# Kernel optimization log

Measured on AMD Instinct MI355X. Metric: run time of the kernel, lower is better.

The kernel has to match this reference:

```python
import jax, jax.numpy as jnp
import numpy as np

B, N, L, H, D = 4, 256, 4, 256, 128  # batch, nodes, labels, hidden, hidden//2
DEG = 16                              # neighbors per (label, node) row (fixed by construction)
M = L * DEG                           # == max_neighbor in the torch code (total degree)


def setup_inputs() -> dict:
    key = jax.random.key(0)
    ks = jax.random.split(key, 12)
    x = jax.random.normal(ks[0], (B, N, H), dtype=jnp.float32)
    feature = jax.random.normal(ks[1], (B, N, 2), dtype=jnp.float32)
    # adjacency with exactly DEG neighbors per (b, l, k) row -> max_neighbor = L*DEG static
    scores = jax.random.uniform(ks[2], (B, L, N, N), dtype=jnp.float32)
    nb = jnp.argsort(-scores, axis=-1)[..., :DEG]                     # [B,L,N,DEG]
    adj = jax.nn.one_hot(nb, N, dtype=jnp.float32).sum(axis=-2)      # [B,L,N,N] binary
    # parameters
    fc_w = jax.random.normal(ks[3], (H, H + 2), dtype=jnp.float32) / np.sqrt(H + 2)
    fc_b = jnp.zeros((H,), jnp.float32)
    ln_g = jnp.ones((H,), jnp.float32)
    ln_b = jnp.zeros((H,), jnp.float32)
    W = jax.random.normal(ks[4], (L, H, D), dtype=jnp.float32) * np.sqrt(2.0 / (H + D))  # xavier
    w_ih = jax.random.normal(ks[5], (4 * H, D), dtype=jnp.float32) / np.sqrt(H)
    w_hh = jax.random.normal(ks[6], (4 * H, H), dtype=jnp.float32) / np.sqrt(H)
    b_ih = jnp.zeros((4 * H,), jnp.float32)
    b_hh = jnp.zeros((4 * H,), jnp.float32)
    return dict(x=x, feature=feature, adj=adj, fc_w=fc_w, fc_b=fc_b, ln_g=ln_g,
                ln_b=ln_b, W=W, w_ih=w_ih, w_hh=w_hh, b_ih=b_ih, b_hh=b_hh)


def _lstm_last(seq, w_ih, w_hh, b_ih, b_hh):
    # seq: [Bt, T, D]; torch nn.LSTM gate order (i, f, g, o); returns last hidden [Bt, Hh]
    Bt = seq.shape[0]
    Hh = w_hh.shape[1]
    bias = b_ih + b_hh

    def step(carry, xt):
        h, c = carry
        gates = xt @ w_ih.T + h @ w_hh.T + bias          # [Bt, 4H]
        i, f, g, o = jnp.split(gates, 4, axis=-1)
        c = jax.nn.sigmoid(f) * c + jax.nn.sigmoid(i) * jnp.tanh(g)
        h = jax.nn.sigmoid(o) * jnp.tanh(c)
        return (h, c), None

    h0 = jnp.zeros((Bt, Hh), seq.dtype)
    (h, _), _ = jax.lax.scan(step, (h0, h0), jnp.swapaxes(seq, 0, 1))
    return h


def reference(x, feature, adj, fc_w, fc_b, ln_g, ln_b, W, w_ih, w_hh, b_ih, b_hh):
    # fc + layernorm + tanh (dropout: eval mode -> identity)
    h = jnp.concatenate([x, feature], axis=-1) @ fc_w.T + fc_b        # [B,N,H]
    mu = h.mean(-1, keepdims=True)
    var = h.var(-1, keepdims=True)
    h = (h - mu) / jnp.sqrt(var + 1e-5) * ln_g + ln_b
    h = jnp.tanh(h)
    # per-label projection of all node features: xw[b,l,n] = h[b,n] @ W[l]
    xw = jnp.einsum('bnh,lhd->blnd', h, W)                            # [B,L,N,D]
    # packed neighbor indices in ascending node order (argsort is stable; adj binary)
    idx = jnp.argsort(1.0 - adj, axis=-1)[..., :DEG]                  # [B,L,N,DEG]
    neigh = jnp.take_along_axis(xw[:, :, None, :, :], idx[..., None], axis=3)  # [B,L,N,DEG,D]
    # torch fills only first deg slots per label, zero-pads to max_neighbor = M
    supports = jnp.pad(neigh, ((0, 0), (0, 0), (0, 0), (0, M - DEG), (0, 0)))  # [B,L,N,M,D]
    supports = jnp.transpose(supports, (0, 2, 1, 3, 4)).reshape(-1, M, xw.shape[-1])  # [B*N*L,M,D]
    last = _lstm_last(supports, w_ih, w_hh, b_ih, b_hh).reshape(h.shape[0], h.shape[1], L, -1)
    out = h + last.mean(axis=2)
    return out + h   # returned dict['x'] = 2*h + mean(supports)
```

## Files before the change

### kernel.cpp

```cpp
#include <hip/hip_runtime.h>
#include <hip/hip_bf16.h>
#include <math.h>

#define B_ 4
#define N_ 256
#define L_ 4
#define H_ 256
#define D_ 128
#define DEG_ 16
#define T_ 64

#define OFF_H     0
#define OFF_FCWT  262144
#define OFF_BIAS  328192
#define OFF_IDX   329216
#define OFF_XWB   394752
#define OFF_PHH   656896
#define OFF_PIH   787968
#define OFF_HG    853504
#define OFF_CTR   1902080

typedef __attribute__((ext_vector_type(8))) short short8;
typedef __attribute__((ext_vector_type(4))) float f32x4;

__device__ __forceinline__ float sigf(float x)  { return 1.f / (1.f + __expf(-x)); }
__device__ __forceinline__ float tanhf_(float x){ return 2.f / (1.f + __expf(-2.f * x)) - 1.f; }
__device__ __forceinline__ unsigned short f2b(float f) {
    __hip_bfloat16 h = __float2bfloat16(f);
    return __builtin_bit_cast(unsigned short, h);
}
__device__ __forceinline__ float b2f(unsigned short s) {
    unsigned int u = ((unsigned int)s) << 16;
    return __builtin_bit_cast(float, u);
}
__device__ __forceinline__ f32x4 splat4(float v) { f32x4 r; r[0]=v; r[1]=v; r[2]=v; r[3]=v; return r; }

__global__ void k_prep(const float* __restrict__ fc_w, const float* __restrict__ w_ih,
                       const float* __restrict__ w_hh, const float* __restrict__ b_ih,
                       const float* __restrict__ b_hh, float* __restrict__ ws) {
    int i = blockIdx.x * blockDim.x + threadIdx.x;
    unsigned short* phh = (unsigned short*)(ws + OFF_PHH);
    unsigned short* pih = (unsigned short*)(ws + OFF_PIH);
    if (i < 256) ((int*)(ws + OFF_CTR))[i] = 0;
    if (i < 66048) {
        int k = i >> 8, j = i & 255;
        ws[OFF_FCWT + i] = fc_w[j * 258 + k];
    } else if (i < 66048 + 262144) {
        int p = i - 66048;
        int j = p & 7, lane = (p >> 3) & 63, kt = (p >> 9) & 7, nt = (p >> 12) & 3, w = (p >> 14) & 7, slc = (p >> 17) & 1;
        int n = nt * 256 + slc * 128 + w * 16 + (lane & 15);
        int k = kt * 32 + (lane >> 4) * 8 + j;
        phh[p] = f2b(w_hh[n * 256 + k]);
    } else if (i < 66048 + 262144 + 131072) {
        int p = i - (66048 + 262144);
        int j = p & 7, lane = (p >> 3) & 63, kt = (p >> 9) & 3, nt = (p >> 11) & 3, w = (p >> 13) & 7, slc = (p >> 16) & 1;
        int n = nt * 256 + slc * 128 + w * 16 + (lane & 15);
        int k = kt * 32 + (lane >> 4) * 8 + j;
        pih[p] = f2b(w_ih[n * 128 + k]);
    } else if (i < 66048 + 262144 + 131072 + 1024) {
        int u = i - (66048 + 262144 + 131072);
        ws[OFF_BIAS + u] = b_ih[u] + b_hh[u];
    }
}

__global__ void k_fc_ln(const float* __restrict__ x, const float* __restrict__ feat,
                        const float* __restrict__ fc_b, const float* __restrict__ ln_g,
                        const float* __restrict__ ln_b, float* __restrict__ ws) {
    __shared__ float inl[260];
    __shared__ float r1[256], r2[256];
    int row = blockIdx.x, tid = threadIdx.x;
    inl[tid] = x[row * H_ + tid];
    if (tid < 2) inl[H_ + tid] = feat[row * 2 + tid];
    __syncthreads();
    const float* fcwT = ws + OFF_FCWT;
    float acc = fc_b[tid];
    #pragma unroll 4
    for (int k = 0; k < 258; ++k) acc += fcwT[k * 256 + tid] * inl[k];
    r1[tid] = acc; r2[tid] = acc * acc;
    __syncthreads();
    for (int o = 128; o > 0; o >>= 1) {
        if (tid < o) { r1[tid] += r1[tid + o]; r2[tid] += r2[tid + o]; }
        __syncthreads();
    }
    float mu  = r1[0] * (1.f / 256.f);
    float var = r2[0] * (1.f / 256.f) - mu * mu;
    float v = (acc - mu) * rsqrtf(var + 1e-5f) * ln_g[tid] + ln_b[tid];
    ws[OFF_H + row * H_ + tid] = tanhf_(v);
}

__global__ void k_xw(const float* __restrict__ Wm, float* __restrict__ ws) {
    __shared__ float hs[32 * 256];
    int bid = blockIdx.x;
    int tile = bid & 7, l = (bid >> 3) & 3, b = bid >> 5;
    int n0 = tile * 32, tid = threadIdx.x;
    const float* hsrc = ws + OFF_H + (b * N_ + n0) * H_;
    for (int i = tid * 4; i < 32 * 256; i += 256 * 4)
        *(float4*)&hs[i] = *(const float4*)&hsrc[i];
    __syncthreads();
    int r0 = (tid >> 5) * 4, c0 = (tid & 31) * 4;
    float acc[4][4] = {};
    const float* wl = Wm + l * H_ * D_;
    for (int k = 0; k < 256; ++k) {
        float4 wv = *(const float4*)&wl[k * D_ + c0];
        #pragma unroll
        for (int r = 0; r < 4; ++r) {
            float hv = hs[(r0 + r) * 256 + k];
            acc[r][0] += hv * wv.x; acc[r][1] += hv * wv.y;
            acc[r][2] += hv * wv.z; acc[r][3] += hv * wv.w;
        }
    }
    unsigned short* xwb = (unsigned short*)(ws + OFF_XWB);
    #pragma unroll
    for (int r = 0; r < 4; ++r) {
        unsigned int lo = (unsigned int)f2b(acc[r][0]) | ((unsigned int)f2b(acc[r][1]) << 16);
        unsigned int hi = (unsigned int)f2b(acc[r][2]) | ((unsigned int)f2b(acc[r][3]) << 16);
        uint2 v; v.x = lo; v.y = hi;
        *(uint2*)&xwb[((b * L_ + l) * N_ + (n0 + r0 + r)) * D_ + c0] = v;
    }
}

__global__ void k_idx(const float* __restrict__ adj, float* __restrict__ ws) {
    int row = blockIdx.x;
    int tid = threadIdx.x;
    __shared__ int wc[4];
    bool a = adj[row * N_ + tid] > 0.5f;
    unsigned long long m = __ballot(a);
    int lane = tid & 63, w = tid >> 6;
    if (lane == 0) wc[w] = __popcll(m);
    __syncthreads();
    int base = 0;
    for (int i = 0; i < w; ++i) base += wc[i];
    int pos = base + __popcll(m & ((1ull << lane) - 1ull));
    int* idxb = (int*)(ws + OFF_IDX);
    if (a && pos < DEG_) idxb[row * DEG_ + pos] = tid;
}

__global__ __launch_bounds__(512, 2)
void k_lstm2(float* __restrict__ out, float* __restrict__ ws) {
    __shared__ __align__(16) unsigned short wih_s[65536];
    __shared__ __align__(16) unsigned short hbuf[32 * 256];
    __shared__ int idx_s[32 * 16];
    const int tid = threadIdx.x;
    const int lane = tid & 63, w = tid >> 6;
    const int c15 = lane & 15, lg = lane >> 4;
    const int bid = blockIdx.x;
    const int g = (bid & 7) | ((bid >> 4) << 3);
    const int slc = (bid >> 3) & 1;
    const int partner = bid ^ 8;
    const int gs0 = g * 32;

    const unsigned short* phh = (const unsigned short*)(ws + OFF_PHH);
    const unsigned short* pih = (const unsigned short*)(ws + OFF_PIH);
    const float* bias = ws + OFF_BIAS;
    const int* idxb = (const int*)(ws + OFF_IDX);
    const unsigned short* xwb = (const unsigned short*)(ws + OFF_XWB);
    unsigned short* hg = (unsigned short*)(ws + OFF_HG);
    int* ctr = (int*)(ws + OFF_CTR);

    {
        const uint4* src = (const uint4*)(pih + slc * 65536);
        uint4* dst = (uint4*)wih_s;
        for (int i = tid; i < 8192; i += 512) dst[i] = src[i];
    }
    for (int i = tid; i < 4096; i += 512) ((unsigned int*)hbuf)[i] = 0;
    {
        int sl = tid >> 4, tt = tid & 15;
        int gsq = gs0 + sl;
        int bbx = gsq >> 10, nn = (gsq >> 2) & 255, ll = gsq & 3;
        idx_s[sl * 16 + tt] = idxb[(((bbx << 2) + ll) * 256 + nn) * DEG_ + tt];
    }

    short8 WH[4][8];
    const short8* ph8 = (const short8*)phh;
    #pragma unroll
    for (int nt = 0; nt < 4; ++nt)
        #pragma unroll
        for (int kt = 0; kt < 8; ++kt)
            WH[nt][kt] = ph8[(((slc * 8 + w) * 32) + nt * 8 + kt) * 64 + lane];

    float bb4[4];
    #pragma unroll
    for (int nt = 0; nt < 4; ++nt) bb4[nt] = bias[nt * 256 + slc * 128 + w * 16 + c15];

    int xbb[2];
    #pragma unroll
    for (int m = 0; m < 2; ++m) {
        int gsq = gs0 + m * 16 + c15;
        int bbx = gsq >> 10, ll = gsq & 3;
        xbb[m] = ((bbx << 2) + ll) * 256;
    }

    float cst[2][4];
    #pragma unroll
    for (int m = 0; m < 2; ++m)
        #pragma unroll
        for (int r = 0; r < 4; ++r) cst[m][r] = 0.f;

    const int sr = tid >> 4, sch = tid & 15;
    const int slcP = 1 - slc;

    __syncthreads();

    for (int t = 0; t < T_; ++t) {
        const int cur = t & 1, nxt = cur ^ 1;
        if (t > 0) {
            if (tid == 0) {
                while (__hip_atomic_load(ctr + partner, __ATOMIC_RELAXED, __HIP_MEMORY_SCOPE_AGENT) < t)
                    __builtin_amdgcn_s_sleep(1);
            }
            __syncthreads();
            {
                const unsigned long long* src = (const unsigned long long*)
                    (hg + ((long)(g * 2 + cur) * 32 + sr) * 256 + slcP * 128 + sch * 8);
                unsigned long long v0 = __hip_atomic_load(src,     __ATOMIC_RELAXED, __HIP_MEMORY_SCOPE_AGENT);
                unsigned long long v1 = __hip_atomic_load(src + 1, __ATOMIC_RELAXED, __HIP_MEMORY_SCOPE_AGENT);
                unsigned short* d = hbuf + sr * 256 + (((slcP * 16 + sch) ^ (sr & 7)) * 8);
                *(unsigned long long*)d = v0;
                *(unsigned long long*)(d + 4) = v1;
            }
            __syncthreads();
        }

        float hv[2][4];
        #pragma unroll
        for (int m = 0; m < 2; ++m) {
            short8 hA[8];
            #pragma unroll
            for (int kt = 0; kt < 8; ++kt)
                hA[kt] = *(const short8*)&hbuf[(m * 16 + c15) * 256 + (((kt * 4 + lg) ^ (c15 & 7)) * 8)];
            short8 xA[4];
            if (t < DEG_) {
                int nb = idx_s[(m * 16 + c15) * 16 + t];
                const short8* s8 = (const short8*)(xwb + (xbb[m] + nb) * D_);
                #pragma unroll
                for (int kt = 0; kt < 4; ++kt) xA[kt] = s8[kt * 4 + lg];
            }
            f32x4 acc[4];
            #pragma unroll
            for (int nt = 0; nt < 4; ++nt) {
                acc[nt] = splat4(bb4[nt]);
                #pragma unroll
                for (int kt = 0; kt < 8; ++kt)
                    acc[nt] = __builtin_amdgcn_mfma_f32_16x16x32_bf16(hA[kt], WH[nt][kt], acc[nt], 0, 0, 0);
                if (t < DEG_) {
                    #pragma unroll
                    for (int kt = 0; kt < 4; ++kt) {
                        short8 wf = *(const short8*)&wih_s[(((w * 4 + nt) * 4 + kt) * 64 + lane) * 8];
                        acc[nt] = __builtin_amdgcn_mfma_f32_16x16x32_bf16(xA[kt], wf, acc[nt], 0, 0, 0);
                    }
                }
            }
            #pragma unroll
            for (int r = 0; r < 4; ++r) {
                float gi = sigf(acc[0][r]);
                float gf = sigf(acc[1][r]);
                float gg = tanhf_(acc[2][r]);
                float go = sigf(acc[3][r]);
                float cc = gf * cst[m][r] + gi * gg;
                cst[m][r] = cc;
                hv[m][r] = go * tanhf_(cc);
            }
        }
        __syncthreads();
        #pragma unroll
        for (int m = 0; m < 2; ++m)
            #pragma unroll
            for (int r = 0; r < 4; ++r) {
                int row = m * 16 + lg * 4 + r;
                int cu = slc * 128 + w * 16 + c15;
                int chunk = (cu >> 3) ^ (row & 7);
                hbuf[row * 256 + chunk * 8 + (c15 & 7)] = f2b(hv[m][r]);
            }
        __syncthreads();
        if (t < T_ - 1) {
            const unsigned short* s = hbuf + sr * 256 + (((slc * 16 + sch) ^ (sr & 7)) * 8);
            unsigned long long v0 = *(const unsigned long long*)s;
            unsigned long long v1 = *(const unsigned long long*)(s + 4);
            unsigned long long* d = (unsigned long long*)
                (hg + ((long)(g * 2 + nxt) * 32 + sr) * 256 + slc * 128 + sch * 8);
            __hip_atomic_store(d,     v0, __ATOMIC_RELAXED, __HIP_MEMORY_SCOPE_AGENT);
            __hip_atomic_store(d + 1, v1, __ATOMIC_RELAXED, __HIP_MEMORY_SCOPE_AGENT);
            __syncthreads();
            if (tid == 0)
                __hip_atomic_store(ctr + bid, t + 1, __ATOMIC_RELAXED, __HIP_MEMORY_SCOPE_AGENT);
        }
    }

    const float* hln = ws + OFF_H;
    const int p = tid >> 6, uu = tid & 63;
    const int bn = g * 8 + p;
    #pragma unroll
    for (int j = 0; j < 2; ++j) {
        int cu = slc * 128 + j * 64 + uu;
        float ssum = 0.f;
        #pragma unroll
        for (int l2 = 0; l2 < 4; ++l2) {
            int s = p * 4 + l2;
            ssum += b2f(hbuf[s * 256 + (((cu >> 3) ^ (s & 7)) * 8) + (cu & 7)]);
        }
        int gi = bn * 256 + cu;
        out[gi] = 2.f * hln[gi] + 0.25f * ssum;
    }
}

extern "C" void kernel_launch(void* const* d_in, const int* in_sizes, int n_in,
                              void* d_out, int out_size, void* d_ws, size_t ws_size,
                              hipStream_t stream) {
    const float* x    = (const float*)d_in[0];
    const float* feat = (const float*)d_in[1];
    const float* adj  = (const float*)d_in[2];
    const float* fc_w = (const float*)d_in[3];
    const float* fc_b = (const float*)d_in[4];
    const float* ln_g = (const float*)d_in[5];
    const float* ln_b = (const float*)d_in[6];
    const float* Wm   = (const float*)d_in[7];
    const float* w_ih = (const float*)d_in[8];
    const float* w_hh = (const float*)d_in[9];
    const float* b_ih = (const float*)d_in[10];
    const float* b_hh = (const float*)d_in[11];
    float* ws  = (float*)d_ws;
    float* out = (float*)d_out;

    hipLaunchKernelGGL(k_prep,   dim3(1798), dim3(256), 0, stream, fc_w, w_ih, w_hh, b_ih, b_hh, ws);
    hipLaunchKernelGGL(k_fc_ln,  dim3(1024), dim3(256), 0, stream, x, feat, fc_b, ln_g, ln_b, ws);
    hipLaunchKernelGGL(k_xw,     dim3(128),  dim3(256), 0, stream, Wm, ws);
    hipLaunchKernelGGL(k_idx,    dim3(4096), dim3(256), 0, stream, adj, ws);
    hipLaunchKernelGGL(k_lstm2,  dim3(256),  dim3(512), 0, stream, out, ws);
}
```

Baseline: 411.1 us.

## Read partner half of hidden state directly from global, drop LDS staging barrier

Each block of the pair no longer copies the partner's half of the hidden state into shared memory behind an extra barrier each step. It loads those four K-tiles straight from the global exchange buffer into MFMA operands, and rotates the W_hh K-tile order so its own half comes from LDS. This removes one __syncthreads and an LDS round trip per timestep on the serial LSTM critical path. In exchange, the exchange buffer and counters are zeroed with a memset so step-0 global reads are valid, which adds an extra memset launch.

```diff
diff --git a/kernel.cpp b/kernel.cpp
--- a/kernel.cpp
+++ b/kernel.cpp
@@ -35,13 +35,19 @@
 }
 __device__ __forceinline__ f32x4 splat4(float v) { f32x4 r; r[0]=v; r[1]=v; r[2]=v; r[3]=v; return r; }
 
+__device__ __forceinline__ short8 ld_hg16(const unsigned short* p) {
+    union { unsigned long long q[2]; short8 s; } u;
+    u.q[0] = __hip_atomic_load((const unsigned long long*)p,     __ATOMIC_RELAXED, __HIP_MEMORY_SCOPE_AGENT);
+    u.q[1] = __hip_atomic_load(((const unsigned long long*)p) + 1, __ATOMIC_RELAXED, __HIP_MEMORY_SCOPE_AGENT);
+    return u.s;
+}
+
 __global__ void k_prep(const float* __restrict__ fc_w, const float* __restrict__ w_ih,
                        const float* __restrict__ w_hh, const float* __restrict__ b_ih,
                        const float* __restrict__ b_hh, float* __restrict__ ws) {
     int i = blockIdx.x * blockDim.x + threadIdx.x;
     unsigned short* phh = (unsigned short*)(ws + OFF_PHH);
     unsigned short* pih = (unsigned short*)(ws + OFF_PIH);
-    if (i < 256) ((int*)(ws + OFF_CTR))[i] = 0;
     if (i < 66048) {
         int k = i >> 8, j = i & 255;
         ws[OFF_FCWT + i] = fc_w[j * 258 + k];
@@ -147,6 +153,7 @@
     const int g = (bid & 7) | ((bid >> 4) << 3);
     const int slc = (bid >> 3) & 1;
     const int partner = bid ^ 8;
+    const int ktO = slc * 4;
     const int gs0 = g * 32;
 
     const unsigned short* phh = (const unsigned short*)(ws + OFF_PHH);
@@ -175,8 +182,10 @@
     #pragma unroll
     for (int nt = 0; nt < 4; ++nt)
         #pragma unroll
-        for (int kt = 0; kt < 8; ++kt)
-            WH[nt][kt] = ph8[(((slc * 8 + w) * 32) + nt * 8 + kt) * 64 + lane];
+        for (int kk = 0; kk < 8; ++kk) {
+            int pkt = (ktO + kk) & 7;
+            WH[nt][kk] = ph8[(((slc * 8 + w) * 32) + nt * 8 + pkt) * 64 + lane];
+        }
 
     float bb4[4];
     #pragma unroll
@@ -189,6 +198,7 @@
         int bbx = gsq >> 10, ll = gsq & 3;
         xbb[m] = ((bbx << 2) + ll) * 256;
     }
+    const int slcP = 1 - slc;
 
     float cst[2][4];
     #pragma unroll
@@ -197,7 +207,6 @@
         for (int r = 0; r < 4; ++r) cst[m][r] = 0.f;
 
     const int sr = tid >> 4, sch = tid & 15;
-    const int slcP = 1 - slc;
 
     __syncthreads();
 
@@ -209,25 +218,21 @@
                     __builtin_amdgcn_s_sleep(1);
             }
             __syncthreads();
-            {
-                const unsigned long long* src = (const unsigned long long*)
-                    (hg + ((long)(g * 2 + cur) * 32 + sr) * 256 + slcP * 128 + sch * 8);
-                unsigned long long v0 = __hip_atomic_load(src,     __ATOMIC_RELAXED, __HIP_MEMORY_SCOPE_AGENT);
-                unsigned long long v1 = __hip_atomic_load(src + 1, __ATOMIC_RELAXED, __HIP_MEMORY_SCOPE_AGENT);
-                unsigned short* d = hbuf + sr * 256 + (((slcP * 16 + sch) ^ (sr & 7)) * 8);
-                *(unsigned long long*)d = v0;
-                *(unsigned long long*)(d + 4) = v1;
-            }
-            __syncthreads();
         }
 
         float hv[2][4];
         #pragma unroll
         for (int m = 0; m < 2; ++m) {
             short8 hA[8];
+            {
+                const unsigned short* prow = hg + ((long)(g * 2 + cur) * 32 + (m * 16 + c15)) * 256 + slcP * 128;
+                #pragma unroll
+                for (int kk = 4; kk < 8; ++kk)
+                    hA[kk] = ld_hg16(prow + ((kk - 4) * 4 + lg) * 8);
+            }
             #pragma unroll
-            for (int kt = 0; kt < 8; ++kt)
-                hA[kt] = *(const short8*)&hbuf[(m * 16 + c15) * 256 + (((kt * 4 + lg) ^ (c15 & 7)) * 8)];
+            for (int kk = 0; kk < 4; ++kk)
+                hA[kk] = *(const short8*)&hbuf[(m * 16 + c15) * 256 + ((((ktO + kk) * 4 + lg) ^ (c15 & 7)) * 8)];
             short8 xA[4];
             if (t < DEG_) {
                 int nb = idx_s[(m * 16 + c15) * 16 + t];
@@ -240,8 +245,8 @@
             for (int nt = 0; nt < 4; ++nt) {
                 acc[nt] = splat4(bb4[nt]);
                 #pragma unroll
-                for (int kt = 0; kt < 8; ++kt)
-                    acc[nt] = __builtin_amdgcn_mfma_f32_16x16x32_bf16(hA[kt], WH[nt][kt], acc[nt], 0, 0, 0);
+                for (int kk = 0; kk < 8; ++kk)
+                    acc[nt] = __builtin_amdgcn_mfma_f32_16x16x32_bf16(hA[kk], WH[nt][kk], acc[nt], 0, 0, 0);
                 if (t < DEG_) {
                     #pragma unroll
                     for (int kt = 0; kt < 4; ++kt) {
@@ -321,6 +326,8 @@
     float* ws  = (float*)d_ws;
     float* out = (float*)d_out;
 
+    hipMemsetAsync((char*)d_ws + (size_t)OFF_HG * 4, 0,
+                   (size_t)(OFF_CTR + 256 - OFF_HG) * 4, stream);
     hipLaunchKernelGGL(k_prep,   dim3(1798), dim3(256), 0, stream, fc_w, w_ih, w_hh, b_ih, b_hh, ws);
     hipLaunchKernelGGL(k_fc_ln,  dim3(1024), dim3(256), 0, stream, x, feat, fc_b, ln_g, ln_b, ws);
     hipLaunchKernelGGL(k_xw,     dim3(128),  dim3(256), 0, stream, Wm, ws);
```

New measurement: 563.7 us. 37.1% more time.

## Fuse neighbor-index extraction into LSTM kernel and split recurrence loop

Applied to the files above, without the earlier changes.

Drops the separate k_idx launch and builds each row's packed neighbor indices inside the LSTM kernel, using wave ballots over the adjacency rows. The time loop is split into a first phase with input projection (t<DEG) and a second phase without it, which removes the per-step branch. Each thread now writes its hidden values straight to global memory before the LDS write, so the extra copy pass and the barrier before the partner signal go away. The cost is more adjacency reads at the start of the LSTM kernel, and the partner sync now depends on element-wise relaxed atomic stores followed by barriers.

```diff
diff --git a/kernel.cpp b/kernel.cpp
--- a/kernel.cpp
+++ b/kernel.cpp
@@ -13,7 +13,6 @@
 #define OFF_H     0
 #define OFF_FCWT  262144
 #define OFF_BIAS  328192
-#define OFF_IDX   329216
 #define OFF_XWB   394752
 #define OFF_PHH   656896
 #define OFF_PIH   787968
@@ -119,24 +118,8 @@
     }
 }
 
-__global__ void k_idx(const float* __restrict__ adj, float* __restrict__ ws) {
-    int row = blockIdx.x;
-    int tid = threadIdx.x;
-    __shared__ int wc[4];
-    bool a = adj[row * N_ + tid] > 0.5f;
-    unsigned long long m = __ballot(a);
-    int lane = tid & 63, w = tid >> 6;
-    if (lane == 0) wc[w] = __popcll(m);
-    __syncthreads();
-    int base = 0;
-    for (int i = 0; i < w; ++i) base += wc[i];
-    int pos = base + __popcll(m & ((1ull << lane) - 1ull));
-    int* idxb = (int*)(ws + OFF_IDX);
-    if (a && pos < DEG_) idxb[row * DEG_ + pos] = tid;
-}
-
 __global__ __launch_bounds__(512, 2)
-void k_lstm2(float* __restrict__ out, float* __restrict__ ws) {
+void k_lstm2(const float* __restrict__ adj, float* __restrict__ out, float* __restrict__ ws) {
     __shared__ __align__(16) unsigned short wih_s[65536];
     __shared__ __align__(16) unsigned short hbuf[32 * 256];
     __shared__ int idx_s[32 * 16];
@@ -148,11 +131,10 @@
     const int slc = (bid >> 3) & 1;
     const int partner = bid ^ 8;
     const int gs0 = g * 32;
-
-    const unsigned short* phh = (const unsigned short*)(ws + OFF_PHH);
+    const int cu0 = slc * 128 + w * 16 + c15;
+
     const unsigned short* pih = (const unsigned short*)(ws + OFF_PIH);
     const float* bias = ws + OFF_BIAS;
-    const int* idxb = (const int*)(ws + OFF_IDX);
     const unsigned short* xwb = (const unsigned short*)(ws + OFF_XWB);
     unsigned short* hg = (unsigned short*)(ws + OFF_HG);
     int* ctr = (int*)(ws + OFF_CTR);
@@ -163,15 +145,25 @@
         for (int i = tid; i < 8192; i += 512) dst[i] = src[i];
     }
     for (int i = tid; i < 4096; i += 512) ((unsigned int*)hbuf)[i] = 0;
-    {
-        int sl = tid >> 4, tt = tid & 15;
+    #pragma unroll
+    for (int q = 0; q < 4; ++q) {
+        int sl = w * 4 + q;
         int gsq = gs0 + sl;
         int bbx = gsq >> 10, nn = (gsq >> 2) & 255, ll = gsq & 3;
-        idx_s[sl * 16 + tt] = idxb[(((bbx << 2) + ll) * 256 + nn) * DEG_ + tt];
+        const float* arow = adj + ((size_t)((((bbx << 2) + ll) * 256 + nn))) * 256;
+        int base = 0;
+        #pragma unroll
+        for (int j = 0; j < 4; ++j) {
+            bool a = arow[j * 64 + lane] > 0.5f;
+            unsigned long long mb = __ballot(a);
+            int rank = base + __popcll(mb & ((1ull << lane) - 1ull));
+            if (a && rank < DEG_) idx_s[sl * DEG_ + rank] = j * 64 + lane;
+            base += __popcll(mb);
+        }
     }
 
     short8 WH[4][8];
-    const short8* ph8 = (const short8*)phh;
+    const short8* ph8 = (const short8*)((const unsigned short*)(ws + OFF_PHH));
     #pragma unroll
     for (int nt = 0; nt < 4; ++nt)
         #pragma unroll
@@ -180,7 +172,7 @@
 
     float bb4[4];
     #pragma unroll
-    for (int nt = 0; nt < 4; ++nt) bb4[nt] = bias[nt * 256 + slc * 128 + w * 16 + c15];
+    for (int nt = 0; nt < 4; ++nt) bb4[nt] = bias[nt * 256 + cu0];
 
     int xbb[2];
     #pragma unroll
@@ -201,7 +193,7 @@
 
     __syncthreads();
 
-    for (int t = 0; t < T_; ++t) {
+    for (int t = 0; t < DEG_; ++t) {
         const int cur = t & 1, nxt = cur ^ 1;
         if (t > 0) {
             if (tid == 0) {
@@ -229,7 +221,7 @@
             for (int kt = 0; kt < 8; ++kt)
                 hA[kt] = *(const short8*)&hbuf[(m * 16 + c15) * 256 + (((kt * 4 + lg) ^ (c15 & 7)) * 8)];
             short8 xA[4];
-            if (t < DEG_) {
+            {
                 int nb = idx_s[(m * 16 + c15) * 16 + t];
                 const short8* s8 = (const short8*)(xwb + (xbb[m] + nb) * D_);
                 #pragma unroll
@@ -242,12 +234,10 @@
                 #pragma unroll
                 for (int kt = 0; kt < 8; ++kt)
                     acc[nt] = __builtin_amdgcn_mfma_f32_16x16x32_bf16(hA[kt], WH[nt][kt], acc[nt], 0, 0, 0);
-                if (t < DEG_) {
-                    #pragma unroll
-                    for (int kt = 0; kt < 4; ++kt) {
-                        short8 wf = *(const short8*)&wih_s[(((w * 4 + nt) * 4 + kt) * 64 + lane) * 8];
-                        acc[nt] = __builtin_amdgcn_mfma_f32_16x16x32_bf16(xA[kt], wf, acc[nt], 0, 0, 0);
-                    }
+                #pragma unroll
+                for (int kt = 0; kt < 4; ++kt) {
+                    short8 wf = *(const short8*)&wih_s[(((w * 4 + nt) * 4 + kt) * 64 + lane) * 8];
+                    acc[nt] = __builtin_amdgcn_mfma_f32_16x16x32_bf16(xA[kt], wf, acc[nt], 0, 0, 0);
                 }
             }
             #pragma unroll
@@ -261,29 +251,94 @@
                 hv[m][r] = go * tanhf_(cc);
             }
         }
+        {
+            unsigned short* hb = hg + ((long)(g * 2 + nxt) * 32) * 256 + cu0;
+            #pragma unroll
+            for (int m = 0; m < 2; ++m)
+                #pragma unroll
+                for (int r = 0; r < 4; ++r)
+                    __hip_atomic_store(hb + (m * 16 + lg * 4 + r) * 256, f2b(hv[m][r]),
+                                       __ATOMIC_RELAXED, __HIP_MEMORY_SCOPE_AGENT);
+        }
         __syncthreads();
         #pragma unroll
         for (int m = 0; m < 2; ++m)
             #pragma unroll
             for (int r = 0; r < 4; ++r) {
                 int row = m * 16 + lg * 4 + r;
-                int cu = slc * 128 + w * 16 + c15;
-                int chunk = (cu >> 3) ^ (row & 7);
+                int chunk = (cu0 >> 3) ^ (row & 7);
                 hbuf[row * 256 + chunk * 8 + (c15 & 7)] = f2b(hv[m][r]);
             }
         __syncthreads();
+        if (tid == 0)
+            __hip_atomic_store(ctr + bid, t + 1, __ATOMIC_RELAXED, __HIP_MEMORY_SCOPE_AGENT);
+    }
+
+    for (int t = DEG_; t < T_; ++t) {
+        const int cur = t & 1, nxt = cur ^ 1;
+        if (tid == 0) {
+            while (__hip_atomic_load(ctr + partner, __ATOMIC_RELAXED, __HIP_MEMORY_SCOPE_AGENT) < t)
+                __builtin_amdgcn_s_sleep(1);
+        }
+        __syncthreads();
+        {
+            const unsigned long long* src = (const unsigned long long*)
+                (hg + ((long)(g * 2 + cur) * 32 + sr) * 256 + slcP * 128 + sch * 8);
+            unsigned long long v0 = __hip_atomic_load(src,     __ATOMIC_RELAXED, __HIP_MEMORY_SCOPE_AGENT);
+            unsigned long long v1 = __hip_atomic_load(src + 1, __ATOMIC_RELAXED, __HIP_MEMORY_SCOPE_AGENT);
+            unsigned short* d = hbuf + sr * 256 + (((slcP * 16 + sch) ^ (sr & 7)) * 8);
+            *(unsigned long long*)d = v0;
+            *(unsigned long long*)(d + 4) = v1;
+        }
+        __syncthreads();
+
+        float hv[2][4];
+        #pragma unroll
+        for (int m = 0; m < 2; ++m) {
+            short8 hA[8];
+            #pragma unroll
+            for (int kt = 0; kt < 8; ++kt)
+                hA[kt] = *(const short8*)&hbuf[(m * 16 + c15) * 256 + (((kt * 4 + lg) ^ (c15 & 7)) * 8)];
+            f32x4 acc[4];
+            #pragma unroll
+            for (int nt = 0; nt < 4; ++nt) {
+                acc[nt] = splat4(bb4[nt]);
+                #pragma unroll
+                for (int kt = 0; kt < 8; ++kt)
+                    acc[nt] = __builtin_amdgcn_mfma_f32_16x16x32_bf16(hA[kt], WH[nt][kt], acc[nt], 0, 0, 0);
+            }
+            #pragma unroll
+            for (int r = 0; r < 4; ++r) {
+                float gi = sigf(acc[0][r]);
+                float gf = sigf(acc[1][r]);
+                float gg = tanhf_(acc[2][r]);
+                float go = sigf(acc[3][r]);
+                float cc = gf * cst[m][r] + gi * gg;
+                cst[m][r] = cc;
+                hv[m][r] = go * tanhf_(cc);
+            }
+        }
         if (t < T_ - 1) {
-            const unsigned short* s = hbuf + sr * 256 + (((slc * 16 + sch) ^ (sr & 7)) * 8);
-            unsigned long long v0 = *(const unsigned long long*)s;
-            unsigned long long v1 = *(const unsigned long long*)(s + 4);
-            unsigned long long* d = (unsigned long long*)
-                (hg + ((long)(g * 2 + nxt) * 32 + sr) * 256 + slc * 128 + sch * 8);
-            __hip_atomic_store(d,     v0, __ATOMIC_RELAXED, __HIP_MEMORY_SCOPE_AGENT);
-            __hip_atomic_store(d + 1, v1, __ATOMIC_RELAXED, __HIP_MEMORY_SCOPE_AGENT);
-            __syncthreads();
-            if (tid == 0)
-                __hip_atomic_store(ctr + bid, t + 1, __ATOMIC_RELAXED, __HIP_MEMORY_SCOPE_AGENT);
-        }
+            unsigned short* hb = hg + ((long)(g * 2 + nxt) * 32) * 256 + cu0;
+            #pragma unroll
+            for (int m = 0; m < 2; ++m)
+                #pragma unroll
+                for (int r = 0; r < 4; ++r)
+                    __hip_atomic_store(hb + (m * 16 + lg * 4 + r) * 256, f2b(hv[m][r]),
+                                       __ATOMIC_RELAXED, __HIP_MEMORY_SCOPE_AGENT);
+        }
+        __syncthreads();
+        #pragma unroll
+        for (int m = 0; m < 2; ++m)
+            #pragma unroll
+            for (int r = 0; r < 4; ++r) {
+                int row = m * 16 + lg * 4 + r;
+                int chunk = (cu0 >> 3) ^ (row & 7);
+                hbuf[row * 256 + chunk * 8 + (c15 & 7)] = f2b(hv[m][r]);
+            }
+        __syncthreads();
+        if (tid == 0 && t < T_ - 1)
+            __hip_atomic_store(ctr + bid, t + 1, __ATOMIC_RELAXED, __HIP_MEMORY_SCOPE_AGENT);
     }
 
     const float* hln = ws + OFF_H;
@@ -324,6 +379,5 @@
     hipLaunchKernelGGL(k_prep,   dim3(1798), dim3(256), 0, stream, fc_w, w_ih, w_hh, b_ih, b_hh, ws);
     hipLaunchKernelGGL(k_fc_ln,  dim3(1024), dim3(256), 0, stream, x, feat, fc_b, ln_g, ln_b, ws);
     hipLaunchKernelGGL(k_xw,     dim3(128),  dim3(256), 0, stream, Wm, ws);
-    hipLaunchKernelGGL(k_idx,    dim3(4096), dim3(256), 0, stream, adj, ws);
-    hipLaunchKernelGGL(k_lstm2,  dim3(256),  dim3(512), 0, stream, out, ws);
-}
+    hipLaunchKernelGGL(k_lstm2,  dim3(256),  dim3(512), 0, stream, adj, out, ws);
+}
```

After: 781.7 us. +90.2%, slower.
